# Performance work log

Hardware: AMD Instinct MI355X
Metric: run time of the kernel (lower is better)

Reference implementation:

```python
import jax, jax.numpy as jnp
import numpy as np

B, P, K = 32, 2048, 16
NHID, NCLS = 128, 10

def setup_inputs() -> dict:
    key = jax.random.key(0)
    ks = jax.random.split(key, 8)
    def w(k, shape):
        fan_in = shape[0]
        return jax.random.normal(k, shape, jnp.float32) / np.sqrt(fan_in)
    pos = jax.random.normal(ks[0], (B * P, 3), jnp.float32)
    batch = jnp.repeat(jnp.arange(B, dtype=jnp.int32), P)
    return dict(
        pos=pos, batch=batch,
        W1a=w(ks[1], (3 + 3, NHID)), b1a=jnp.zeros((NHID,), jnp.float32),
        W1b=w(ks[2], (NHID, NHID)), b1b=jnp.zeros((NHID,), jnp.float32),
        W2a=w(ks[3], (NHID + 3, NHID)), b2a=jnp.zeros((NHID,), jnp.float32),
        W2b=w(ks[4], (NHID, NHID)), b2b=jnp.zeros((NHID,), jnp.float32),
        Wc=w(ks[5], (NHID, NCLS)), bc=jnp.zeros((NCLS,), jnp.float32),
    )

def _gather(x, idx):
    # x: [B,P,C], idx: [B,P,K] -> [B,P,K,C]
    return jax.vmap(lambda xb, ib: xb[ib])(x, idx)

def _knn(posb):
    # posb: [B,P,3]; k nearest (incl. self, loop=True) per node -> [B,P,K]
    sq = jnp.sum(posb * posb, axis=-1)                      # [B,P]
    d2 = sq[:, :, None] + sq[:, None, :] - 2.0 * jnp.einsum('bpd,bqd->bpq', posb, posb)
    _, nbr = jax.lax.top_k(-d2, K)                          # [B,P,K]
    return nbr

def _pointnet_layer(h, posb, nbr, Wa, ba, Wb, bb):
    # message: concat(h_j, pos_j - pos_i) -> Linear -> ReLU -> Linear; aggr = max over K
    h_j = _gather(h, nbr)                                   # [B,P,K,C]
    rel = _gather(posb, nbr) - posb[:, :, None, :]          # [B,P,K,3]
    m = jnp.concatenate([h_j, rel], axis=-1)                # [B,P,K,C+3]
    m = jax.nn.relu(jnp.einsum('bpkc,cd->bpkd', m, Wa) + ba)
    m = jnp.einsum('bpkc,cd->bpkd', m, Wb) + bb
    return jnp.max(m, axis=2)                               # [B,P,NHID]

def reference(pos, batch, W1a, b1a, W1b, b1b, W2a, b2a, W2b, b2b, Wc, bc):
    posb = pos.reshape(B, P, 3)                             # batch is sorted, equal-size graphs
    nbr = _knn(posb)
    h = jax.nn.relu(_pointnet_layer(posb, posb, nbr, W1a, b1a, W1b, b1b))
    h = jax.nn.relu(_pointnet_layer(h, posb, nbr, W2a, b2a, W2b, b2b))
    g = jnp.max(h, axis=1)                                  # global_max_pool -> [B,NHID]
    return g @ Wc + bc                                      # [B,NCLS]
```

## Files before the change

kernel.cpp:

```cpp
#include <hip/hip_runtime.h>


typedef __bf16 bf16x8 __attribute__((ext_vector_type(8)));
typedef float  f32x4  __attribute__((ext_vector_type(4)));

#define LDSA __attribute__((aligned(16)))
#define WAVE_LDS_SYNC() __asm__ volatile("s_waitcnt lgkmcnt(0)" ::: "memory")

__global__ __launch_bounds__(512, 4) void knn_kernel(const float* __restrict__ pos,
                                                     int* __restrict__ nbr) {
  __shared__ LDSA float4 P4[2048];
  const int blk = blockIdx.x;
  const int b = blk >> 5;
  const int tid = threadIdx.x;
  const size_t bbase = (size_t)b * 2048;
  for (int idx = tid; idx < 2048; idx += 512) {
    const float* pp = pos + (bbase + idx) * 3;
    float x = pp[0], y = pp[1], z = pp[2];
    P4[idx] = make_float4(x, y, z, fmaf(z, z, fmaf(y, y, x * x)));
  }
  __syncthreads();
  const int wave = tid >> 6, lane = tid & 63;
  const int p0 = (blk & 31) * 64 + wave * 8;
  const unsigned long long below = (1ull << lane) - 1ull;
  const float FINF = __uint_as_float(0x7F800000u);
  for (int it = 0; it < 8; ++it) {
    const int pl = p0 + it;
    const float4 P = P4[pl];
    float m1 = FINF, m2 = FINF, m3 = FINF, m4 = FINF;
    unsigned s1 = 0, s2 = 0, s3 = 0;
#pragma unroll 8
    for (int i = 0; i < 32; ++i) {
      int c = lane + (i << 6);
      float4 Q = P4[c];
      float d2 = (P.w + Q.w) - 2.0f * fmaf(P.z, Q.z, fmaf(P.y, Q.y, P.x * Q.x));
      bool c1 = d2 < m1, c2 = d2 < m2, c3 = d2 < m3;
      float nm4 = __builtin_amdgcn_fmed3f(m3, m4, d2);
      float nm3 = __builtin_amdgcn_fmed3f(m2, m3, d2);
      float nm2 = __builtin_amdgcn_fmed3f(m1, m2, d2);
      float nm1 = fminf(m1, d2);
      s3 = c2 ? s2 : (c3 ? (unsigned)c : s3);
      s2 = c1 ? s1 : (c2 ? (unsigned)c : s2);
      s1 = c1 ? (unsigned)c : s1;
      m1 = nm1; m2 = nm2; m3 = nm3; m4 = nm4;
    }
    unsigned k1 = __float_as_uint(m1); k1 = ((int)k1 < 0) ? ~k1 : (k1 | 0x80000000u);
    unsigned k2 = __float_as_uint(m2); k2 = ((int)k2 < 0) ? ~k2 : (k2 | 0x80000000u);
    unsigned k3 = __float_as_uint(m3); k3 = ((int)k3 < 0) ? ~k3 : (k3 | 0x80000000u);
    unsigned k4 = __float_as_uint(m4); k4 = ((int)k4 < 0) ? ~k4 : (k4 | 0x80000000u);
    unsigned v = 0;
#pragma unroll
    for (int bit = 31; bit >= 0; --bit) {
      unsigned t = v | (1u << bit);
      int cnt = __popcll(__ballot(k1 < t)) + __popcll(__ballot(k2 < t)) +
                __popcll(__ballot(k3 < t));
      if (cnt < 16) v = t;
    }
    const unsigned V = v;
    const long long outbase = ((long long)bbase + pl) * 16;
    if (__any(k4 < V)) {
      unsigned long long K1 = ((unsigned long long)k1 << 32) | s1;
      unsigned long long K2 = ((unsigned long long)k2 << 32) | s2;
      unsigned long long K3 = ((unsigned long long)k3 << 32) | s3;
      unsigned long long lastk = 0;
      for (int r = 0; r < 16; ++r) {
        unsigned long long k = K1, kmin = K1;
#pragma unroll
        for (int off = 1; off < 64; off <<= 1) {
          unsigned long long o = __shfl_xor(kmin, off);
          kmin = (o < kmin) ? o : kmin;
        }
        if (lane == r) nbr[outbase + r] = (int)(kmin & 0xFFFFFFFFull);
        if (k == kmin) { lastk = k; K1 = K2; K2 = K3; K3 = ~0ull; }
        if (r < 15 && __any(K1 == ~0ull)) {
          if (K1 == ~0ull) {
            unsigned long long best = ~0ull;
            for (int i = 0; i < 32; ++i) {
              int c = lane + (i << 6);
              float4 Q = P4[c];
              float d2 = (P.w + Q.w) - 2.0f * fmaf(P.z, Q.z, fmaf(P.y, Q.y, P.x * Q.x));
              unsigned u = __float_as_uint(d2);
              u = ((int)u < 0) ? ~u : (u | 0x80000000u);
              unsigned long long kc = ((unsigned long long)u << 32) | (unsigned)c;
              bool ok = (kc > lastk) & (kc < best);
              best = ok ? kc : best;
            }
            K1 = best;
          }
        }
      }
    } else {
      unsigned long long L1 = __ballot(k1 < V), L2 = __ballot(k2 < V), L3 = __ballot(k3 < V);
      unsigned long long E1 = __ballot(k1 == V), E2 = __ballot(k2 == V), E3 = __ballot(k3 == V);
      int cA = __popcll(L1), cB = cA + __popcll(L2), cT = cB + __popcll(L3);
      int eA = __popcll(E1), eB = eA + __popcll(E2);
      {
        bool lt = k1 < V, eq = k1 == V;
        int plt = __popcll(L1 & below);
        int peq = cT + __popcll(E1 & below);
        int p = lt ? plt : peq;
        if (lt || (eq && peq < 16)) nbr[outbase + p] = (int)s1;
      }
      {
        bool lt = k2 < V, eq = k2 == V;
        int plt = cA + __popcll(L2 & below);
        int peq = cT + eA + __popcll(E2 & below);
        int p = lt ? plt : peq;
        if (lt || (eq && peq < 16)) nbr[outbase + p] = (int)s2;
      }
      {
        bool lt = k3 < V, eq = k3 == V;
        int plt = cB + __popcll(L3 & below);
        int peq = cT + eB + __popcll(E3 & below);
        int p = lt ? plt : peq;
        if (lt || (eq && peq < 16)) nbr[outbase + p] = (int)s3;
      }
    }
  }
}

__global__ __launch_bounds__(256, 2) void layer1_kernel(
    const float* __restrict__ pos, const int* __restrict__ nbr,
    const float* __restrict__ W1a, const float* __restrict__ b1a,
    const float* __restrict__ W1b, const float* __restrict__ b1b,
    __bf16* __restrict__ h1e) {
  __shared__ LDSA char smem[34816];
  __bf16* Wbt = (__bf16*)smem;
  const int tid = threadIdx.x;
  for (int idx = tid; idx < 16384; idx += 256) {
    int k = idx >> 7, n = idx & 127;
    int byteoff = n * 272 + ((k * 2) ^ (((n >> 3) & 7) << 4));
    *(__bf16*)((char*)Wbt + byteoff) = (__bf16)W1b[idx];
  }
  __syncthreads();
  const int wave = tid >> 6, lane = tid & 63;
  const int q = lane >> 4, c15 = lane & 15;
  bf16x8 bfr[8][4];
#pragma unroll
  for (int nt = 0; nt < 8; ++nt)
#pragma unroll
    for (int t = 0; t < 4; ++t) {
      int row = nt * 16 + c15;
      int rbyte = row * 272 + (((t * 32 + q * 8) * 2) ^ (((row >> 3) & 7) << 4));
      bfr[nt][t] = *(const bf16x8*)((const char*)Wbt + rbyte);
    }
  __syncthreads();
  __bf16* mt = (__bf16*)smem + wave * 2176;
  float* base = (float*)(smem + 17408) + wave * 128;
  const int cb = lane & 7, k0 = lane >> 3, C0 = cb * 16;
  float4 s0h[4], s1h[4], s2h[4];
#pragma unroll
  for (int i = 0; i < 4; ++i) {
    float4 a0 = *(const float4*)&W1a[      C0 + 4 * i], r0 = *(const float4*)&W1a[384 + C0 + 4 * i];
    float4 a1 = *(const float4*)&W1a[128 + C0 + 4 * i], r1 = *(const float4*)&W1a[512 + C0 + 4 * i];
    float4 a2 = *(const float4*)&W1a[256 + C0 + 4 * i], r2 = *(const float4*)&W1a[640 + C0 + 4 * i];
    s0h[i] = make_float4(a0.x + r0.x, a0.y + r0.y, a0.z + r0.z, a0.w + r0.w);
    s1h[i] = make_float4(a1.x + r1.x, a1.y + r1.y, a1.z + r1.z, a1.w + r1.w);
    s2h[i] = make_float4(a2.x + r2.x, a2.y + r2.y, a2.z + r2.z, a2.w + r2.w);
  }
  const int c2 = lane * 2;
  const float br0a = W1a[384 + c2], br0b = W1a[384 + c2 + 1];
  const float br1a = W1a[512 + c2], br1b = W1a[512 + c2 + 1];
  const float br2a = W1a[640 + c2], br2b = W1a[640 + c2 + 1];
  const float ba0 = b1a[c2], ba1 = b1a[c2 + 1];
  const float bbi0 = b1b[q * 32 + c15], bbi1 = b1b[q * 32 + 16 + c15];
  const int blk = blockIdx.x, b = blk >> 5;
  const size_t bbase = (size_t)b * 2048;
  const int p0 = (blk & 31) * 64 + wave * 16;
  size_t node = bbase + p0;
  int j0 = nbr[node * 16 + k0];
  int j1 = nbr[node * 16 + k0 + 8];
  float px = pos[node * 3], py = pos[node * 3 + 1], pz = pos[node * 3 + 2];
  for (int it = 0; it < 16; ++it) {
    const int j0c = j0, j1c = j1;
    const float xp = px, yp = py, zp = pz;
    const size_t nodec = node;
    if (it < 15) {
      node = nodec + 1;
      j0 = nbr[node * 16 + k0];
      j1 = nbr[node * 16 + k0 + 8];
      px = pos[node * 3]; py = pos[node * 3 + 1]; pz = pos[node * 3 + 2];
    }
    const float* pj0 = pos + (bbase + j0c) * 3;
    const float* pj1 = pos + (bbase + j1c) * 3;
    const float xa = pj0[0], ya = pj0[1], za = pj0[2];
    const float xb = pj1[0], yb = pj1[1], zb = pj1[2];
    float v0 = ba0 - fmaf(xp, br0a, fmaf(yp, br1a, zp * br2a));
    float v1 = ba1 - fmaf(xp, br0b, fmaf(yp, br1b, zp * br2b));
    *(float2*)&base[c2] = make_float2(v0, v1);
    WAVE_LDS_SYNC();
    float4 bb[4];
#pragma unroll
    for (int i = 0; i < 4; ++i) bb[i] = *(const float4*)&base[C0 + 4 * i];
#pragma unroll
    for (int r = 0; r < 2; ++r) {
      const float xj = r ? xb : xa, yj = r ? yb : ya, zj = r ? zb : za;
      bf16x8 o0, o1;
#pragma unroll
      for (int i = 0; i < 4; ++i) {
        float mx = fmaf(xj, s0h[i].x, fmaf(yj, s1h[i].x, fmaf(zj, s2h[i].x, bb[i].x)));
        float my = fmaf(xj, s0h[i].y, fmaf(yj, s1h[i].y, fmaf(zj, s2h[i].y, bb[i].y)));
        float mz = fmaf(xj, s0h[i].z, fmaf(yj, s1h[i].z, fmaf(zj, s2h[i].z, bb[i].z)));
        float mw = fmaf(xj, s0h[i].w, fmaf(yj, s1h[i].w, fmaf(zj, s2h[i].w, bb[i].w)));
        __bf16 e0 = (__bf16)fmaxf(mx, 0.f), e1 = (__bf16)fmaxf(my, 0.f);
        __bf16 e2 = (__bf16)fmaxf(mz, 0.f), e3 = (__bf16)fmaxf(mw, 0.f);
        if (i < 2) { o0[i * 4 + 0] = e0; o0[i * 4 + 1] = e1; o0[i * 4 + 2] = e2; o0[i * 4 + 3] = e3; }
        else { o1[(i - 2) * 4 + 0] = e0; o1[(i - 2) * 4 + 1] = e1; o1[(i - 2) * 4 + 2] = e2; o1[(i - 2) * 4 + 3] = e3; }
      }
      __bf16* dst = &mt[(k0 + 8 * r) * 136 + C0];
      *(bf16x8*)dst = o0;
      *(bf16x8*)(dst + 8) = o1;
    }
    WAVE_LDS_SYNC();
    bf16x8 af[4];
#pragma unroll
    for (int t = 0; t < 4; ++t)
      af[t] = *(const bf16x8*)&mt[c15 * 136 + t * 32 + q * 8];
    f32x4 acc[8] = {};
#pragma unroll
    for (int nt = 0; nt < 8; ++nt)
#pragma unroll
      for (int t = 0; t < 4; ++t)
        acc[nt] = __builtin_amdgcn_mfma_f32_16x16x32_bf16(af[t], bfr[nt][t], acc[nt], 0, 0, 0);
#pragma unroll
    for (int nt = 0; nt < 8; ++nt) {
      float m4 = fmaxf(fmaxf(acc[nt][0], acc[nt][1]), fmaxf(acc[nt][2], acc[nt][3]));
      m4 = fmaxf(m4, __shfl_xor(m4, 16));
      m4 = fmaxf(m4, __shfl_xor(m4, 32));
      if ((nt >> 1) == q) {
        float bias = (nt & 1) ? bbi1 : bbi0;
        h1e[nodec * 160 + nt * 16 + c15] = (__bf16)fmaxf(m4 + bias, 0.f);
      }
    }
    if (lane < 32) {
      __bf16 v = (__bf16)0.f;
      if (lane == 0) v = (__bf16)xp;
      else if (lane == 1) v = (__bf16)yp;
      else if (lane == 2) v = (__bf16)zp;
      h1e[nodec * 160 + 128 + lane] = v;
    }
  }
}

__global__ __launch_bounds__(256) void mid_gemm_kernel(
    const __bf16* __restrict__ h1e, const float* __restrict__ W2a,
    const float* __restrict__ b2a, __bf16* __restrict__ u2p) {
  __shared__ LDSA __bf16 Wt[128 * 168];
  const int tid = threadIdx.x;
  uint4 z = make_uint4(0, 0, 0, 0);
  for (int idx = tid; idx < 2688; idx += 256) ((uint4*)Wt)[idx] = z;
  __syncthreads();
  for (int idx = tid; idx < 131 * 32; idx += 256) {
    int k = idx >> 5, c4 = (idx & 31) * 4;
    float4 w = *(const float4*)&W2a[k * 128 + c4];
    Wt[(c4 + 0) * 168 + k] = (__bf16)w.x;
    Wt[(c4 + 1) * 168 + k] = (__bf16)w.y;
    Wt[(c4 + 2) * 168 + k] = (__bf16)w.z;
    Wt[(c4 + 3) * 168 + k] = (__bf16)w.w;
  }
  const int wave = tid >> 6, lane = tid & 63;
  const int q = lane >> 4, c15 = lane & 15;
  float biasr[8];
#pragma unroll
  for (int nt = 0; nt < 8; ++nt) biasr[nt] = b2a[nt * 16 + c15];
  __syncthreads();
  for (int tile = 0; tile < 4; ++tile) {
    const int row0 = blockIdx.x * 256 + tile * 64 + wave * 16;
    bf16x8 af[5];
#pragma unroll
    for (int t = 0; t < 5; ++t)
      af[t] = *(const bf16x8*)(h1e + (size_t)(row0 + c15) * 160 + t * 32 + q * 8);
    f32x4 acc[8] = {};
#pragma unroll
    for (int nt = 0; nt < 8; ++nt)
#pragma unroll
      for (int t = 0; t < 5; ++t) {
        bf16x8 bf = *(const bf16x8*)&Wt[(nt * 16 + c15) * 168 + t * 32 + q * 8];
        acc[nt] = __builtin_amdgcn_mfma_f32_16x16x32_bf16(af[t], bf, acc[nt], 0, 0, 0);
      }
#pragma unroll
    for (int nt = 0; nt < 8; ++nt) {
#pragma unroll
      for (int r = 0; r < 4; ++r)
        u2p[(size_t)(row0 + q * 4 + r) * 128 + nt * 16 + c15] = (__bf16)(acc[nt][r] + biasr[nt]);
    }
  }
}

__global__ __launch_bounds__(256, 2) void layer2_kernel(
    const float* __restrict__ pos, const int* __restrict__ nbr,
    const __bf16* __restrict__ u2p, const float* __restrict__ W2a,
    const float* __restrict__ W2b, const float* __restrict__ b2b,
    int* __restrict__ gG) {
  __shared__ LDSA char smem[34816];
  __shared__ int gpart[128];
  __bf16* Wbt = (__bf16*)smem;
  const int tid = threadIdx.x;
  for (int idx = tid; idx < 16384; idx += 256) {
    int k = idx >> 7, n = idx & 127;
    int byteoff = n * 272 + ((k * 2) ^ (((n >> 3) & 7) << 4));
    *(__bf16*)((char*)Wbt + byteoff) = (__bf16)W2b[idx];
  }
  if (tid < 128) gpart[tid] = 0;
  __syncthreads();
  const int wave = tid >> 6, lane = tid & 63;
  const int q = lane >> 4, c15 = lane & 15;
  bf16x8 bfr[8][4];
#pragma unroll
  for (int nt = 0; nt < 8; ++nt)
#pragma unroll
    for (int t = 0; t < 4; ++t) {
      int row = nt * 16 + c15;
      int rbyte = row * 272 + (((t * 32 + q * 8) * 2) ^ (((row >> 3) & 7) << 4));
      bfr[nt][t] = *(const bf16x8*)((const char*)Wbt + rbyte);
    }
  __syncthreads();
  __bf16* mt = (__bf16*)smem + wave * 2176;
  float* proj = (float*)(smem + 17408) + wave * 128;
  const int cb = lane & 7, k0 = lane >> 3, C0 = cb * 16;
  const int c2 = lane * 2;
  const float r0a = W2a[16384 + c2], r0b = W2a[16384 + c2 + 1];
  const float r1a = W2a[16512 + c2], r1b = W2a[16512 + c2 + 1];
  const float r2a = W2a[16640 + c2], r2b = W2a[16640 + c2 + 1];
  const float bbi0 = b2b[q * 32 + c15], bbi1 = b2b[q * 32 + 16 + c15];
  const int lb = blockIdx.x;
  const int xcd = lb & 7, slot = lb >> 3;
  const int b = xcd + 8 * (slot >> 5);
  const int bi = slot & 31;
  const size_t bbase = (size_t)b * 2048;
  const int p0 = bi * 64 + wave * 16;
  size_t node = bbase + p0;
  int j0 = nbr[node * 16 + k0];
  int j1 = nbr[node * 16 + k0 + 8];
  float px = pos[node * 3], py = pos[node * 3 + 1], pz = pos[node * 3 + 2];
  for (int it = 0; it < 16; ++it) {
    const int j0c = j0, j1c = j1;
    const float xp = px, yp = py, zp = pz;
    const size_t nodec = node;
    if (it < 15) {
      node = nodec + 1;
      j0 = nbr[node * 16 + k0];
      j1 = nbr[node * 16 + k0 + 8];
      px = pos[node * 3]; py = pos[node * 3 + 1]; pz = pos[node * 3 + 2];
    }
    const __bf16* ur0 = u2p + (size_t)(bbase + j0c) * 128 + C0;
    const __bf16* ur1 = u2p + (size_t)(bbase + j1c) * 128 + C0;
    bf16x8 ua0 = *(const bf16x8*)ur0, ua1 = *(const bf16x8*)(ur0 + 8);
    bf16x8 ub0 = *(const bf16x8*)ur1, ub1 = *(const bf16x8*)(ur1 + 8);
    float v0 = fmaf(xp, r0a, fmaf(yp, r1a, zp * r2a));
    float v1 = fmaf(xp, r0b, fmaf(yp, r1b, zp * r2b));
    *(float2*)&proj[c2] = make_float2(v0, v1);
    WAVE_LDS_SYNC();
    float pj[16];
#pragma unroll
    for (int i = 0; i < 4; ++i) *(float4*)&pj[4 * i] = *(const float4*)&proj[C0 + 4 * i];
#pragma unroll
    for (int r = 0; r < 2; ++r) {
      bf16x8 u0 = r ? ub0 : ua0, u1 = r ? ub1 : ua1;
      bf16x8 o0, o1;
#pragma unroll
      for (int e = 0; e < 8; ++e) o0[e] = (__bf16)fmaxf((float)u0[e] - pj[e], 0.f);
#pragma unroll
      for (int e = 0; e < 8; ++e) o1[e] = (__bf16)fmaxf((float)u1[e] - pj[8 + e], 0.f);
      __bf16* dst = &mt[(k0 + 8 * r) * 136 + C0];
      *(bf16x8*)dst = o0;
      *(bf16x8*)(dst + 8) = o1;
    }
    WAVE_LDS_SYNC();
    bf16x8 af[4];
#pragma unroll
    for (int t = 0; t < 4; ++t)
      af[t] = *(const bf16x8*)&mt[c15 * 136 + t * 32 + q * 8];
    f32x4 acc[8] = {};
#pragma unroll
    for (int nt = 0; nt < 8; ++nt)
#pragma unroll
      for (int t = 0; t < 4; ++t)
        acc[nt] = __builtin_amdgcn_mfma_f32_16x16x32_bf16(af[t], bfr[nt][t], acc[nt], 0, 0, 0);
#pragma unroll
    for (int nt = 0; nt < 8; ++nt) {
      float m4 = fmaxf(fmaxf(acc[nt][0], acc[nt][1]), fmaxf(acc[nt][2], acc[nt][3]));
      m4 = fmaxf(m4, __shfl_xor(m4, 16));
      m4 = fmaxf(m4, __shfl_xor(m4, 32));
      if ((nt >> 1) == q) {
        float bias = (nt & 1) ? bbi1 : bbi0;
        float h = fmaxf(m4 + bias, 0.f);
        atomicMax(&gpart[nt * 16 + c15], __float_as_int(h));
      }
    }
  }
  __syncthreads();
  if (tid < 128) atomicMax(&gG[b * 128 + tid], gpart[tid]);
}

__global__ __launch_bounds__(64) void cls_kernel(const int* __restrict__ gG,
                                                 const float* __restrict__ Wc,
                                                 const float* __restrict__ bc,
                                                 float* __restrict__ out) {
  const int b = blockIdx.x, lane = threadIdx.x;
  float g1 = __int_as_float(gG[b * 128 + lane]);
  float g2 = __int_as_float(gG[b * 128 + 64 + lane]);
  float accn[10];
#pragma unroll
  for (int n = 0; n < 10; ++n)
    accn[n] = g1 * Wc[lane * 10 + n] + g2 * Wc[(64 + lane) * 10 + n];
#pragma unroll
  for (int n = 0; n < 10; ++n) {
#pragma unroll
    for (int off = 32; off >= 1; off >>= 1) accn[n] += __shfl_xor(accn[n], off);
  }
  if (lane == 0) {
#pragma unroll
    for (int n = 0; n < 10; ++n) out[b * 10 + n] = accn[n] + bc[n];
  }
}

extern "C" void kernel_launch(void* const* d_in, const int* in_sizes, int n_in,
                              void* d_out, int out_size, void* d_ws, size_t ws_size,
                              hipStream_t stream) {
  const float* pos = (const float*)d_in[0];
  const float* W1a = (const float*)d_in[2];
  const float* b1a = (const float*)d_in[3];
  const float* W1b = (const float*)d_in[4];
  const float* b1b = (const float*)d_in[5];
  const float* W2a = (const float*)d_in[6];
  const float* b2a = (const float*)d_in[7];
  const float* W2b = (const float*)d_in[8];
  const float* b2b = (const float*)d_in[9];
  const float* Wc  = (const float*)d_in[10];
  const float* bc  = (const float*)d_in[11];

  char* ws = (char*)d_ws;
  int*    nbr = (int*)ws;
  __bf16* h1e = (__bf16*)(ws + 4194304);
  __bf16* u2p = (__bf16*)(ws + 25165824);
  int*    gG  = (int*)(ws + 41943040);
  float*  out = (float*)d_out;

  hipMemsetAsync(gG, 0, 32 * 128 * sizeof(int), stream);
  knn_kernel<<<1024, 512, 0, stream>>>(pos, nbr);
  layer1_kernel<<<1024, 256, 0, stream>>>(pos, nbr, W1a, b1a, W1b, b1b, h1e);
  mid_gemm_kernel<<<256, 256, 0, stream>>>(h1e, W2a, b2a, u2p);
  layer2_kernel<<<1024, 256, 0, stream>>>(pos, nbr, u2p, W2a, W2b, b2b, gG);
  cls_kernel<<<32, 64, 0, stream>>>(gG, Wc, bc, out);
}
```

Before: 331.3 us.

## Prefetch neighbor gathers one iteration ahead and drop third-slot index tracking in kNN

In the kNN kernel, the per-candidate index tracking for the third-smallest distance is removed from the hot loop. When that slot might be needed, a second pass over the candidates recovers its index by exact bit-match. In both pointnet layer kernels, the neighbor position and feature gathers are software-pipelined so the next iteration's loads are issued before the MFMA work of the current one. The cost is extra registers and an occasional rescan of all candidates. Bit-match recovery could also pick the wrong index if two candidates have identical distances.

```diff
diff --git a/kernel.cpp b/kernel.cpp
--- a/kernel.cpp
+++ b/kernel.cpp
@@ -28,18 +28,17 @@
     const int pl = p0 + it;
     const float4 P = P4[pl];
     float m1 = FINF, m2 = FINF, m3 = FINF, m4 = FINF;
-    unsigned s1 = 0, s2 = 0, s3 = 0;
+    unsigned s1 = 0, s2 = 0;
 #pragma unroll 8
     for (int i = 0; i < 32; ++i) {
       int c = lane + (i << 6);
       float4 Q = P4[c];
       float d2 = (P.w + Q.w) - 2.0f * fmaf(P.z, Q.z, fmaf(P.y, Q.y, P.x * Q.x));
-      bool c1 = d2 < m1, c2 = d2 < m2, c3 = d2 < m3;
+      bool c1 = d2 < m1, c2 = d2 < m2;
       float nm4 = __builtin_amdgcn_fmed3f(m3, m4, d2);
       float nm3 = __builtin_amdgcn_fmed3f(m2, m3, d2);
       float nm2 = __builtin_amdgcn_fmed3f(m1, m2, d2);
       float nm1 = fminf(m1, d2);
-      s3 = c2 ? s2 : (c3 ? (unsigned)c : s3);
       s2 = c1 ? s1 : (c2 ? (unsigned)c : s2);
       s1 = c1 ? (unsigned)c : s1;
       m1 = nm1; m2 = nm2; m3 = nm3; m4 = nm4;
@@ -57,6 +56,17 @@
       if (cnt < 16) v = t;
     }
     const unsigned V = v;
+    unsigned s3 = 0;
+    if (__any(k3 <= V)) {
+      const unsigned m3b = __float_as_uint(m3);
+#pragma unroll 8
+      for (int i = 0; i < 32; ++i) {
+        int c = lane + (i << 6);
+        float4 Q = P4[c];
+        float d2 = (P.w + Q.w) - 2.0f * fmaf(P.z, Q.z, fmaf(P.y, Q.y, P.x * Q.x));
+        if (__float_as_uint(d2) == m3b) s3 = (unsigned)c;
+      }
+    }
     const long long outbase = ((long long)bbase + pl) * 16;
     if (__any(k4 < V)) {
       unsigned long long K1 = ((unsigned long long)k1 << 32) | s1;
@@ -171,8 +181,11 @@
   int j0 = nbr[node * 16 + k0];
   int j1 = nbr[node * 16 + k0 + 8];
   float px = pos[node * 3], py = pos[node * 3 + 1], pz = pos[node * 3 + 2];
+  const float* pj0p = pos + (bbase + j0) * 3;
+  const float* pj1p = pos + (bbase + j1) * 3;
+  float xa = pj0p[0], ya = pj0p[1], za = pj0p[2];
+  float xb = pj1p[0], yb = pj1p[1], zb = pj1p[2];
   for (int it = 0; it < 16; ++it) {
-    const int j0c = j0, j1c = j1;
     const float xp = px, yp = py, zp = pz;
     const size_t nodec = node;
     if (it < 15) {
@@ -181,10 +194,6 @@
       j1 = nbr[node * 16 + k0 + 8];
       px = pos[node * 3]; py = pos[node * 3 + 1]; pz = pos[node * 3 + 2];
     }
-    const float* pj0 = pos + (bbase + j0c) * 3;
-    const float* pj1 = pos + (bbase + j1c) * 3;
-    const float xa = pj0[0], ya = pj0[1], za = pj0[2];
-    const float xb = pj1[0], yb = pj1[1], zb = pj1[2];
     float v0 = ba0 - fmaf(xp, br0a, fmaf(yp, br1a, zp * br2a));
     float v1 = ba1 - fmaf(xp, br0b, fmaf(yp, br1b, zp * br2b));
     *(float2*)&base[c2] = make_float2(v0, v1);
@@ -210,6 +219,12 @@
       __bf16* dst = &mt[(k0 + 8 * r) * 136 + C0];
       *(bf16x8*)dst = o0;
       *(bf16x8*)(dst + 8) = o1;
+    }
+    if (it < 15) {
+      const float* q0 = pos + (bbase + j0) * 3;
+      const float* q1 = pos + (bbase + j1) * 3;
+      xa = q0[0]; ya = q0[1]; za = q0[2];
+      xb = q1[0]; yb = q1[1]; zb = q1[2];
     }
     WAVE_LDS_SYNC();
     bf16x8 af[4];
@@ -333,8 +348,11 @@
   int j0 = nbr[node * 16 + k0];
   int j1 = nbr[node * 16 + k0 + 8];
   float px = pos[node * 3], py = pos[node * 3 + 1], pz = pos[node * 3 + 2];
+  const __bf16* u0p = u2p + (size_t)(bbase + j0) * 128 + C0;
+  const __bf16* u1p = u2p + (size_t)(bbase + j1) * 128 + C0;
+  bf16x8 ua0 = *(const bf16x8*)u0p, ua1 = *(const bf16x8*)(u0p + 8);
+  bf16x8 ub0 = *(const bf16x8*)u1p, ub1 = *(const bf16x8*)(u1p + 8);
   for (int it = 0; it < 16; ++it) {
-    const int j0c = j0, j1c = j1;
     const float xp = px, yp = py, zp = pz;
     const size_t nodec = node;
     if (it < 15) {
@@ -343,10 +361,6 @@
       j1 = nbr[node * 16 + k0 + 8];
       px = pos[node * 3]; py = pos[node * 3 + 1]; pz = pos[node * 3 + 2];
     }
-    const __bf16* ur0 = u2p + (size_t)(bbase + j0c) * 128 + C0;
-    const __bf16* ur1 = u2p + (size_t)(bbase + j1c) * 128 + C0;
-    bf16x8 ua0 = *(const bf16x8*)ur0, ua1 = *(const bf16x8*)(ur0 + 8);
-    bf16x8 ub0 = *(const bf16x8*)ur1, ub1 = *(const bf16x8*)(ur1 + 8);
     float v0 = fmaf(xp, r0a, fmaf(yp, r1a, zp * r2a));
     float v1 = fmaf(xp, r0b, fmaf(yp, r1b, zp * r2b));
     *(float2*)&proj[c2] = make_float2(v0, v1);
@@ -365,6 +379,12 @@
       __bf16* dst = &mt[(k0 + 8 * r) * 136 + C0];
       *(bf16x8*)dst = o0;
       *(bf16x8*)(dst + 8) = o1;
+    }
+    if (it < 15) {
+      const __bf16* q0 = u2p + (size_t)(bbase + j0) * 128 + C0;
+      const __bf16* q1 = u2p + (size_t)(bbase + j1) * 128 + C0;
+      ua0 = *(const bf16x8*)q0; ua1 = *(const bf16x8*)(q0 + 8);
+      ub0 = *(const bf16x8*)q1; ub1 = *(const bf16x8*)(q1 + 8);
     }
     WAVE_LDS_SYNC();
     bf16x8 af[4];
```

After: 332.2 us. About the same (+0.3%).

## Stream weight fragments from LDS and defer third-neighbor index recovery in kNN

Applied to the files above, without the earlier changes.

In layer1 and layer2, the W-b bf16 fragments (128 VGPRs per lane) are no longer held in registers. They stay resident in a separately swizzled LDS region and are reloaded for each MFMA, which cuts register pressure and may raise occupancy at the cost of more LDS traffic. The per-wave bias/proj scratch is padded to a stride of 20 floats to avoid bank conflicts. In kNN, the third-slot index is dropped from the hot loop and recovered afterwards by a rescan only when needed, trading a rare second pass for a shorter inner loop.

```diff
diff --git a/kernel.cpp b/kernel.cpp
--- a/kernel.cpp
+++ b/kernel.cpp
@@ -28,18 +28,17 @@
     const int pl = p0 + it;
     const float4 P = P4[pl];
     float m1 = FINF, m2 = FINF, m3 = FINF, m4 = FINF;
-    unsigned s1 = 0, s2 = 0, s3 = 0;
+    unsigned s1 = 0, s2 = 0;
 #pragma unroll 8
     for (int i = 0; i < 32; ++i) {
       int c = lane + (i << 6);
       float4 Q = P4[c];
       float d2 = (P.w + Q.w) - 2.0f * fmaf(P.z, Q.z, fmaf(P.y, Q.y, P.x * Q.x));
-      bool c1 = d2 < m1, c2 = d2 < m2, c3 = d2 < m3;
+      bool c1 = d2 < m1, c2 = d2 < m2;
       float nm4 = __builtin_amdgcn_fmed3f(m3, m4, d2);
       float nm3 = __builtin_amdgcn_fmed3f(m2, m3, d2);
       float nm2 = __builtin_amdgcn_fmed3f(m1, m2, d2);
       float nm1 = fminf(m1, d2);
-      s3 = c2 ? s2 : (c3 ? (unsigned)c : s3);
       s2 = c1 ? s1 : (c2 ? (unsigned)c : s2);
       s1 = c1 ? (unsigned)c : s1;
       m1 = nm1; m2 = nm2; m3 = nm3; m4 = nm4;
@@ -57,6 +56,17 @@
       if (cnt < 16) v = t;
     }
     const unsigned V = v;
+    unsigned s3 = 0;
+    if (__any(k3 <= V)) {
+      const unsigned m3b = __float_as_uint(m3);
+#pragma unroll 8
+      for (int i = 0; i < 32; ++i) {
+        int c = lane + (i << 6);
+        float4 Q = P4[c];
+        float d2 = (P.w + Q.w) - 2.0f * fmaf(P.z, Q.z, fmaf(P.y, Q.y, P.x * Q.x));
+        if (__float_as_uint(d2) == m3b) s3 = (unsigned)c;
+      }
+    }
     const long long outbase = ((long long)bbase + pl) * 16;
     if (__any(k4 < V)) {
       unsigned long long K1 = ((unsigned long long)k1 << 32) | s1;
@@ -124,29 +134,19 @@
     const float* __restrict__ W1a, const float* __restrict__ b1a,
     const float* __restrict__ W1b, const float* __restrict__ b1b,
     __bf16* __restrict__ h1e) {
-  __shared__ LDSA char smem[34816];
+  __shared__ LDSA char smem[52736];
   __bf16* Wbt = (__bf16*)smem;
   const int tid = threadIdx.x;
   for (int idx = tid; idx < 16384; idx += 256) {
     int k = idx >> 7, n = idx & 127;
-    int byteoff = n * 272 + ((k * 2) ^ (((n >> 3) & 7) << 4));
+    int byteoff = n * 256 + ((k * 2) ^ ((n & 7) << 4));
     *(__bf16*)((char*)Wbt + byteoff) = (__bf16)W1b[idx];
   }
   __syncthreads();
   const int wave = tid >> 6, lane = tid & 63;
   const int q = lane >> 4, c15 = lane & 15;
-  bf16x8 bfr[8][4];
-#pragma unroll
-  for (int nt = 0; nt < 8; ++nt)
-#pragma unroll
-    for (int t = 0; t < 4; ++t) {
-      int row = nt * 16 + c15;
-      int rbyte = row * 272 + (((t * 32 + q * 8) * 2) ^ (((row >> 3) & 7) << 4));
-      bfr[nt][t] = *(const bf16x8*)((const char*)Wbt + rbyte);
-    }
-  __syncthreads();
-  __bf16* mt = (__bf16*)smem + wave * 2176;
-  float* base = (float*)(smem + 17408) + wave * 128;
+  __bf16* mt = (__bf16*)(smem + 32768) + wave * 2176;
+  float* base = (float*)(smem + 50176) + wave * 160;
   const int cb = lane & 7, k0 = lane >> 3, C0 = cb * 16;
   float4 s0h[4], s1h[4], s2h[4];
 #pragma unroll
@@ -159,6 +159,7 @@
     s2h[i] = make_float4(a2.x + r2.x, a2.y + r2.y, a2.z + r2.z, a2.w + r2.w);
   }
   const int c2 = lane * 2;
+  const int bslot = (lane >> 3) * 20 + (lane & 7) * 2;
   const float br0a = W1a[384 + c2], br0b = W1a[384 + c2 + 1];
   const float br1a = W1a[512 + c2], br1b = W1a[512 + c2 + 1];
   const float br2a = W1a[640 + c2], br2b = W1a[640 + c2 + 1];
@@ -187,11 +188,11 @@
     const float xb = pj1[0], yb = pj1[1], zb = pj1[2];
     float v0 = ba0 - fmaf(xp, br0a, fmaf(yp, br1a, zp * br2a));
     float v1 = ba1 - fmaf(xp, br0b, fmaf(yp, br1b, zp * br2b));
-    *(float2*)&base[c2] = make_float2(v0, v1);
+    *(float2*)&base[bslot] = make_float2(v0, v1);
     WAVE_LDS_SYNC();
     float4 bb[4];
 #pragma unroll
-    for (int i = 0; i < 4; ++i) bb[i] = *(const float4*)&base[C0 + 4 * i];
+    for (int i = 0; i < 4; ++i) bb[i] = *(const float4*)&base[cb * 20 + 4 * i];
 #pragma unroll
     for (int r = 0; r < 2; ++r) {
       const float xj = r ? xb : xa, yj = r ? yb : ya, zj = r ? zb : za;
@@ -220,8 +221,12 @@
 #pragma unroll
     for (int nt = 0; nt < 8; ++nt)
 #pragma unroll
-      for (int t = 0; t < 4; ++t)
-        acc[nt] = __builtin_amdgcn_mfma_f32_16x16x32_bf16(af[t], bfr[nt][t], acc[nt], 0, 0, 0);
+      for (int t = 0; t < 4; ++t) {
+        const int row = nt * 16 + c15;
+        bf16x8 bf = *(const bf16x8*)((const char*)Wbt +
+                     row * 256 + (((t * 32 + q * 8) * 2) ^ ((row & 7) << 4)));
+        acc[nt] = __builtin_amdgcn_mfma_f32_16x16x32_bf16(af[t], bf, acc[nt], 0, 0, 0);
+      }
 #pragma unroll
     for (int nt = 0; nt < 8; ++nt) {
       float m4 = fmaxf(fmaxf(acc[nt][0], acc[nt][1]), fmaxf(acc[nt][2], acc[nt][3]));
@@ -292,33 +297,24 @@
     const __bf16* __restrict__ u2p, const float* __restrict__ W2a,
     const float* __restrict__ W2b, const float* __restrict__ b2b,
     int* __restrict__ gG) {
-  __shared__ LDSA char smem[34816];
+  __shared__ LDSA char smem[52736];
   __shared__ int gpart[128];
   __bf16* Wbt = (__bf16*)smem;
   const int tid = threadIdx.x;
   for (int idx = tid; idx < 16384; idx += 256) {
     int k = idx >> 7, n = idx & 127;
-    int byteoff = n * 272 + ((k * 2) ^ (((n >> 3) & 7) << 4));
+    int byteoff = n * 256 + ((k * 2) ^ ((n & 7) << 4));
     *(__bf16*)((char*)Wbt + byteoff) = (__bf16)W2b[idx];
   }
   if (tid < 128) gpart[tid] = 0;
   __syncthreads();
   const int wave = tid >> 6, lane = tid & 63;
   const int q = lane >> 4, c15 = lane & 15;
-  bf16x8 bfr[8][4];
-#pragma unroll
-  for (int nt = 0; nt < 8; ++nt)
-#pragma unroll
-    for (int t = 0; t < 4; ++t) {
-      int row = nt * 16 + c15;
-      int rbyte = row * 272 + (((t * 32 + q * 8) * 2) ^ (((row >> 3) & 7) << 4));
-      bfr[nt][t] = *(const bf16x8*)((const char*)Wbt + rbyte);
-    }
-  __syncthreads();
-  __bf16* mt = (__bf16*)smem + wave * 2176;
-  float* proj = (float*)(smem + 17408) + wave * 128;
+  __bf16* mt = (__bf16*)(smem + 32768) + wave * 2176;
+  float* proj = (float*)(smem + 50176) + wave * 160;
   const int cb = lane & 7, k0 = lane >> 3, C0 = cb * 16;
   const int c2 = lane * 2;
+  const int bslot = (lane >> 3) * 20 + (lane & 7) * 2;
   const float r0a = W2a[16384 + c2], r0b = W2a[16384 + c2 + 1];
   const float r1a = W2a[16512 + c2], r1b = W2a[16512 + c2 + 1];
   const float r2a = W2a[16640 + c2], r2b = W2a[16640 + c2 + 1];
@@ -349,11 +345,11 @@
     bf16x8 ub0 = *(const bf16x8*)ur1, ub1 = *(const bf16x8*)(ur1 + 8);
     float v0 = fmaf(xp, r0a, fmaf(yp, r1a, zp * r2a));
     float v1 = fmaf(xp, r0b, fmaf(yp, r1b, zp * r2b));
-    *(float2*)&proj[c2] = make_float2(v0, v1);
+    *(float2*)&proj[bslot] = make_float2(v0, v1);
     WAVE_LDS_SYNC();
     float pj[16];
 #pragma unroll
-    for (int i = 0; i < 4; ++i) *(float4*)&pj[4 * i] = *(const float4*)&proj[C0 + 4 * i];
+    for (int i = 0; i < 4; ++i) *(float4*)&pj[4 * i] = *(const float4*)&proj[cb * 20 + 4 * i];
 #pragma unroll
     for (int r = 0; r < 2; ++r) {
       bf16x8 u0 = r ? ub0 : ua0, u1 = r ? ub1 : ua1;
@@ -375,8 +371,12 @@
 #pragma unroll
     for (int nt = 0; nt < 8; ++nt)
 #pragma unroll
-      for (int t = 0; t < 4; ++t)
-        acc[nt] = __builtin_amdgcn_mfma_f32_16x16x32_bf16(af[t], bfr[nt][t], acc[nt], 0, 0, 0);
+      for (int t = 0; t < 4; ++t) {
+        const int row = nt * 16 + c15;
+        bf16x8 bf = *(const bf16x8*)((const char*)Wbt +
+                     row * 256 + (((t * 32 + q * 8) * 2) ^ ((row & 7) << 4)));
+        acc[nt] = __builtin_amdgcn_mfma_f32_16x16x32_bf16(af[t], bf, acc[nt], 0, 0, 0);
+      }
 #pragma unroll
     for (int nt = 0; nt < 8; ++nt) {
       float m4 = fmaxf(fmaxf(acc[nt][0], acc[nt][1]), fmaxf(acc[nt][2], acc[nt][3]));
```

New measurement: 341.4 us. 3.0% more time.
